# Kernel tuning notes

Hardware: AMD Instinct MI355X
Metric: run time of the kernel (lower is better)

## Reference

```python
import jax, jax.numpy as jnp
import numpy as np

B, N, D = 64, 1024, 128
K = 6  # hardcoded neighbor count in the module


def setup_inputs() -> dict:
    key = jax.random.key(0)
    ks = jax.random.split(key, 11)
    def lin(k, out_d, in_d):
        kw, kb = jax.random.split(k)
        s = 1.0 / np.sqrt(in_d)
        W = jax.random.uniform(kw, (out_d, in_d), minval=-s, maxval=s, dtype=jnp.float32)
        b = jax.random.uniform(kb, (out_d,), minval=-s, maxval=s, dtype=jnp.float32)
        return W, b
    loc = jax.random.uniform(ks[0], (B, N, 2), dtype=jnp.float32)
    deadline = jax.random.uniform(ks[1], (B, N), dtype=jnp.float32)
    depot = jax.random.uniform(ks[2], (B, 2), dtype=jnp.float32)
    W3d, b3d = lin(ks[3], D, 3)
    W2d, b2d = lin(ks[4], D, 2)
    Wnb, bnb = lin(ks[5], D, K * D)
    Wdep, bdep = lin(ks[6], D, 2)
    return {"loc": loc, "deadline": deadline, "depot": depot,
            "W3d": W3d, "b3d": b3d, "W2d": W2d, "b2d": b2d,
            "Wnb": Wnb, "bnb": bnb, "Wdep": Wdep, "bdep": bdep}


def reference(loc, deadline, depot, W3d, b3d, W2d, b2d, Wnb, bnb, Wdep, bdep):
    x = jnp.concatenate([loc, deadline[:, :, None]], axis=2)  # [B,N,3]
    x2 = x[:, :, 0:2]                                          # [B,N,2]
    F2 = jnp.einsum('bnf,df->bnd', x2, W2d) + b2d              # [B,N,D]
    F3 = jnp.einsum('bnf,df->bnd', x, W3d) + b3d               # [B,N,D]
    # pairwise euclidean distances; indices are non-differentiable -> stop_gradient
    diff = x2[:, None, :, :] - x2[:, :, None, :]               # [B,N,N,2]
    dist = jnp.sqrt(jnp.sum(diff * diff, axis=-1))             # [B,N,N]
    _, neighbors = jax.lax.top_k(jax.lax.stop_gradient(-dist), K)  # [B,N,K] smallest dists (incl. self)
    # faithful quirk: original does F0_embedding_2d[:, neighbors][0] == gather from batch-0 embeddings
    nb = F2[0][neighbors]                                      # [B,N,K,D]
    nb_c = nb.reshape(nb.shape[0], nb.shape[1], K * nb.shape[3])  # [B,N,K*D]
    Fn = jnp.einsum('bnf,df->bnd', nb_c, Wnb) + bnb            # [B,N,D]
    Ff = Fn + F3
    dep = depot @ Wdep.T + bdep                                 # [B,D]
    h = jax.nn.leaky_relu(jnp.concatenate([dep[:, None, :], Ff], axis=1), negative_slope=0.01)
    return h, h.mean(axis=1)
```

## Files before the change

### kernel.cpp

```cpp
#include <hip/hip_runtime.h>
#include <hip/hip_bf16.h>

#define CB 64
#define CN 1024
#define CD 128
#define CK 6

typedef __attribute__((ext_vector_type(8))) short short8;
typedef __attribute__((ext_vector_type(4))) float floatx4;

__device__ __forceinline__ unsigned short f2bf(float f) {
    union { float f; unsigned u; } c; c.f = f;
    unsigned u = c.u;
    u += 0x7FFFu + ((u >> 16) & 1u);
    return (unsigned short)(u >> 16);
}
__device__ __forceinline__ float bf2f(unsigned short u) {
    union { unsigned u; float f; } c; c.u = ((unsigned)u) << 16; return c.f;
}
__device__ __forceinline__ float bfe(const uint4& g, int dd) {
    unsigned w = (&g.x)[dd >> 1];
    unsigned short h = (dd & 1) ? (unsigned short)(w >> 16)
                                : (unsigned short)(w & 0xFFFFu);
    return bf2f(h);
}

#define WS_G      0
#define WS_NBRS   3145728
#define WS_IDS    3932160
#define WS_STARTS 4063232
#define WS_PART   4129024

struct SortSM { float2 pts[CN]; int cnt[256]; int base[256]; };
struct GSM    { unsigned short As[128 * 40]; unsigned short Bs[128 * 40]; };
union GridSM  { SortSM s; GSM g; };

__global__ void __launch_bounds__(256) k_gridg(
    const float* __restrict__ loc,
    const float* __restrict__ W2d,
    const float* __restrict__ b2d,
    const float* __restrict__ Wnb,
    unsigned short* __restrict__ ids,
    int* __restrict__ starts,
    unsigned short* __restrict__ G16)
{
    __shared__ GridSM sm;
    int t = threadIdx.x;

    if (blockIdx.x < 64) {
        int b = blockIdx.x;
        const float2* lb = (const float2*)loc + b * CN;
#pragma unroll
        for (int r = 0; r < 4; ++r) sm.s.pts[t + r * 256] = lb[t + r * 256];
        sm.s.cnt[t] = 0;
        __syncthreads();
        int mycell[4];
#pragma unroll
        for (int r = 0; r < 4; ++r) {
            float2 p = sm.s.pts[t * 4 + r];
            int cx = (int)(p.x * 16.0f); cx = cx > 15 ? 15 : cx;
            int cy = (int)(p.y * 16.0f); cy = cy > 15 ? 15 : cy;
            mycell[r] = (cy << 4) + cx;
            atomicAdd(&sm.s.cnt[mycell[r]], 1);
        }
        __syncthreads();
        for (int off = 1; off < 256; off <<= 1) {
            int u = (t >= off) ? sm.s.cnt[t - off] : 0;
            __syncthreads();
            sm.s.cnt[t] += u;
            __syncthreads();
        }
        int excl = (t == 0) ? 0 : sm.s.cnt[t - 1];
        sm.s.base[t] = excl;
        starts[b * 257 + t] = excl;
        if (t == 255) starts[b * 257 + 256] = sm.s.cnt[255];
        __syncthreads();
#pragma unroll
        for (int r = 0; r < 4; ++r) {
            int pos = atomicAdd(&sm.s.base[mycell[r]], 1);
            ids[b * CN + pos] = (unsigned short)(t * 4 + r);
        }
        return;
    }

    int gb = blockIdx.x - 64;
    int k = gb % 6;
    int tile = gb / 6;
    int n0 = tile << 7;

    int wave = t >> 6, lane = t & 63;
    int koff = (lane >> 4) * 8;
    int mrow = lane & 15;

    int e2 = t & 15, rg = t >> 4;
    float2 pl[8];
#pragma unroll
    for (int rr = 0; rr < 8; ++rr)
        pl[rr] = ((const float2*)loc)[n0 + rg + rr * 16];

    int bd = t >> 1, bhalf = t & 1;

    floatx4 acc[2][8];
#pragma unroll
    for (int i = 0; i < 2; ++i)
#pragma unroll
        for (int j = 0; j < 8; ++j) acc[i][j] = (floatx4){0.f, 0.f, 0.f, 0.f};

#pragma unroll
    for (int c = 0; c < 4; ++c) {
        __syncthreads();
        {
            int e0 = c * 32 + e2 * 2;
            float wx0 = W2d[e0 * 2],     wy0 = W2d[e0 * 2 + 1], bz0 = b2d[e0];
            float wx1 = W2d[e0 * 2 + 2], wy1 = W2d[e0 * 2 + 3], bz1 = b2d[e0 + 1];
#pragma unroll
            for (int rr = 0; rr < 8; ++rr) {
                float2 p = pl[rr];
                float v0 = fmaf(p.x, wx0, fmaf(p.y, wy0, bz0));
                float v1 = fmaf(p.x, wx1, fmaf(p.y, wy1, bz1));
                unsigned pack = (unsigned)f2bf(v0) | ((unsigned)f2bf(v1) << 16);
                *(unsigned*)&sm.g.As[(rg + rr * 16) * 40 + e2 * 2] = pack;
            }
        }
        {
            const float* src = Wnb + bd * 768 + k * 128 + c * 32 + bhalf * 16;
            float4 f0 = *(const float4*)(src);
            float4 f1 = *(const float4*)(src + 4);
            float4 f2v = *(const float4*)(src + 8);
            float4 f3 = *(const float4*)(src + 12);
            uint4 o0, o1;
            o0.x = (unsigned)f2bf(f0.x) | ((unsigned)f2bf(f0.y) << 16);
            o0.y = (unsigned)f2bf(f0.z) | ((unsigned)f2bf(f0.w) << 16);
            o0.z = (unsigned)f2bf(f1.x) | ((unsigned)f2bf(f1.y) << 16);
            o0.w = (unsigned)f2bf(f1.z) | ((unsigned)f2bf(f1.w) << 16);
            o1.x = (unsigned)f2bf(f2v.x) | ((unsigned)f2bf(f2v.y) << 16);
            o1.y = (unsigned)f2bf(f2v.z) | ((unsigned)f2bf(f2v.w) << 16);
            o1.z = (unsigned)f2bf(f3.x) | ((unsigned)f2bf(f3.y) << 16);
            o1.w = (unsigned)f2bf(f3.z) | ((unsigned)f2bf(f3.w) << 16);
            *(uint4*)&sm.g.Bs[bd * 40 + bhalf * 16] = o0;
            *(uint4*)&sm.g.Bs[bd * 40 + bhalf * 16 + 8] = o1;
        }
        __syncthreads();
        short8 af[2];
#pragma unroll
        for (int i = 0; i < 2; ++i)
            af[i] = *(const short8*)&sm.g.As[(wave * 32 + i * 16 + mrow) * 40 + koff];
#pragma unroll
        for (int j = 0; j < 8; ++j) {
            short8 bfr = *(const short8*)&sm.g.Bs[(j * 16 + mrow) * 40 + koff];
#pragma unroll
            for (int i = 0; i < 2; ++i)
                acc[i][j] = __builtin_amdgcn_mfma_f32_16x16x32_bf16(
                    af[i], bfr, acc[i][j], 0, 0, 0);
        }
    }

    int lq = lane >> 4, lc = lane & 15;
#pragma unroll
    for (int j = 0; j < 8; ++j) {
        int d = j * 16 + lc;
#pragma unroll
        for (int i = 0; i < 2; ++i) {
#pragma unroll
            for (int r = 0; r < 4; ++r) {
                int row = wave * 32 + i * 16 + lq * 4 + r;
                G16[(n0 + row) * 768 + k * 128 + d] = f2bf(acc[i][j][r]);
            }
        }
    }
}

__global__ void __launch_bounds__(256) k_knn(
    const float* __restrict__ loc,
    const unsigned short* __restrict__ ids,
    const int* __restrict__ starts,
    unsigned short* __restrict__ nbrs)
{
    __shared__ float2 xy_tmp[CN];
    __shared__ float2 xy_s[CN];
    __shared__ unsigned short ids_s[CN];
    __shared__ int st_s[257];
    int t = threadIdx.x;
    int b = blockIdx.x >> 4;
    int qbase = (blockIdx.x & 15) << 6;
    const float2* lb = (const float2*)loc + b * CN;
#pragma unroll
    for (int r = 0; r < 4; ++r) {
        int p = t + r * 256;
        xy_tmp[p] = lb[p];
        ids_s[p] = ids[b * CN + p];
    }
    st_s[t] = starts[b * 257 + t];
    if (t == 0) st_s[256] = starts[b * 257 + 256];
    __syncthreads();
#pragma unroll
    for (int r = 0; r < 4; ++r) {
        int p = t + r * 256;
        xy_s[p] = xy_tmp[ids_s[p]];
    }
    __syncthreads();

    int qp = qbase + (t >> 2);
    int pi = t & 3;
    int q = ids_s[qp];
    float2 qxy = xy_s[qp];
    float xq = qxy.x, yq = qxy.y;
    int cx = (int)(xq * 16.0f); cx = cx > 15 ? 15 : cx;
    int cy = (int)(yq * 16.0f); cy = cy > 15 ? 15 : cy;
    float dk[CK]; int ik[CK];
#pragma unroll
    for (int s = 0; s < CK; ++s) { dk[s] = 1e30f; ik[s] = 0x7FFFFFFF; }
    float dk5sq = __builtin_inff();
    const float h = 0.0625f;

#define KNN_CAND(P)                                                        \
    {                                                                      \
        float2 v = xy_s[P];                                                \
        float dx = __fsub_rn(v.x, xq);                                     \
        float dy = __fsub_rn(v.y, yq);                                     \
        float d2 = __fadd_rn(__fmul_rn(dx, dx), __fmul_rn(dy, dy));        \
        if (d2 < dk5sq) {                                                  \
            float ds = __fsqrt_rn(d2);                                     \
            int j = ids_s[P];                                              \
            if (ds < dk[CK - 1] || (ds == dk[CK - 1] && j < ik[CK - 1])) { \
                float dc = ds; int jc = j;                                 \
                _Pragma("unroll")                                          \
                for (int s = 0; s < CK; ++s) {                             \
                    bool sw = (dc < dk[s]) || (dc == dk[s] && jc < ik[s]); \
                    float od = dk[s]; int oi = ik[s];                      \
                    dk[s] = sw ? dc : od; ik[s] = sw ? jc : oi;            \
                    dc = sw ? od : dc;    jc = sw ? oi : jc;               \
                }                                                          \
                if (ik[CK - 1] != 0x7FFFFFFF)                              \
                    dk5sq = __fmul_rn(dk[CK - 1], dk[CK - 1]) * 1.000001f; \
            }                                                              \
        }                                                                  \
    }

    {
        int yl = cy > 0 ? cy - 1 : 0, yh = cy < 15 ? cy + 1 : 15;
        int xl = cx > 0 ? cx - 1 : 0, xh = cx < 15 ? cx + 1 : 15;
        for (int yy = yl; yy <= yh; ++yy) {
            int p  = st_s[(yy << 4) + xl] + pi;
            int pe = st_s[(yy << 4) + xh + 1];
            for (; p < pe; p += 4) KNN_CAND(p)
        }
    }
    bool done;
    {
        int x0 = cx - 1, x1 = cx + 1, y0 = cy - 1, y1 = cy + 1;
        done = (x0 <= 0 && y0 <= 0 && x1 >= 15 && y1 >= 15);
        float mL = x0 > 0  ? __fsub_rn(xq, (float)x0 * h)       : 1e30f;
        float mR = x1 < 15 ? __fsub_rn((float)(x1 + 1) * h, xq) : 1e30f;
        float mB = y0 > 0  ? __fsub_rn(yq, (float)y0 * h)       : 1e30f;
        float mT = y1 < 15 ? __fsub_rn((float)(y1 + 1) * h, yq) : 1e30f;
        float bound = fminf(fminf(mL, mR), fminf(mB, mT)) * 0.999999f;
        done = done || (ik[CK - 1] != 0x7FFFFFFF && dk[CK - 1] < bound);
    }
    if (!done) {
        for (int r = 2; r < 16; ++r) {
            int x0 = cx - r, x1 = cx + r, y0 = cy - r, y1 = cy + r;
            int yl = y0 < 0 ? 0 : y0, yh = y1 > 15 ? 15 : y1;
            int xl = x0 < 0 ? 0 : x0, xh = x1 > 15 ? 15 : x1;
            for (int yy = yl; yy <= yh; ++yy) {
                bool ey = (yy == y0) || (yy == y1);
                if (ey) {
                    int p  = st_s[(yy << 4) + xl] + pi;
                    int pe = st_s[(yy << 4) + xh + 1];
                    for (; p < pe; p += 4) KNN_CAND(p)
                } else {
                    if (x0 >= 0) {
                        int p  = st_s[(yy << 4) + x0] + pi;
                        int pe = st_s[(yy << 4) + x0 + 1];
                        for (; p < pe; p += 4) KNN_CAND(p)
                    }
                    if (x1 <= 15) {
                        int p  = st_s[(yy << 4) + x1] + pi;
                        int pe = st_s[(yy << 4) + x1 + 1];
                        for (; p < pe; p += 4) KNN_CAND(p)
                    }
                }
            }
            if (x0 <= 0 && y0 <= 0 && x1 >= 15 && y1 >= 15) break;
            float mL = x0 > 0  ? __fsub_rn(xq, (float)x0 * h)       : 1e30f;
            float mR = x1 < 15 ? __fsub_rn((float)(x1 + 1) * h, xq) : 1e30f;
            float mB = y0 > 0  ? __fsub_rn(yq, (float)y0 * h)       : 1e30f;
            float mT = y1 < 15 ? __fsub_rn((float)(y1 + 1) * h, yq) : 1e30f;
            float bound = fminf(fminf(mL, mR), fminf(mB, mT)) * 0.999999f;
            if (ik[CK - 1] != 0x7FFFFFFF && dk[CK - 1] < bound) break;
        }
    }
#undef KNN_CAND

#define KNN_MERGE(MASK)                                                     \
    {                                                                       \
        float od[CK]; int oi[CK];                                           \
        _Pragma("unroll")                                                   \
        for (int s = 0; s < CK; ++s) {                                      \
            od[s] = __shfl_xor(dk[s], MASK);                                \
            oi[s] = __shfl_xor(ik[s], MASK);                                \
        }                                                                   \
        _Pragma("unroll")                                                   \
        for (int e = 0; e < CK; ++e) {                                      \
            float dc = od[e]; int jc = oi[e];                               \
            if ((dc < dk[CK - 1]) || (dc == dk[CK - 1] && jc < ik[CK - 1])) { \
                _Pragma("unroll")                                           \
                for (int s = 0; s < CK; ++s) {                              \
                    bool sw = (dc < dk[s]) || (dc == dk[s] && jc < ik[s]);  \
                    float td = dk[s]; int ti = ik[s];                       \
                    dk[s] = sw ? dc : td; ik[s] = sw ? jc : ti;             \
                    dc = sw ? td : dc;    jc = sw ? ti : jc;                \
                }                                                           \
            }                                                               \
        }                                                                   \
    }
    KNN_MERGE(1)
    KNN_MERGE(2)
#undef KNN_MERGE

    if (pi == 0) {
        unsigned short* o = nbrs + (unsigned)(b * CN + q) * CK;
#pragma unroll
        for (int s = 0; s < CK; ++s) o[s] = (unsigned short)ik[s];
    }
}

__global__ void __launch_bounds__(256) k_gather(
    const float* __restrict__ loc,
    const float* __restrict__ dl,
    const unsigned short* __restrict__ nbrs,
    const unsigned short* __restrict__ ids,
    const unsigned short* __restrict__ G16,
    const float* __restrict__ W3d,
    const float* __restrict__ b3d,
    const float* __restrict__ bnb,
    float* __restrict__ outh,
    float* __restrict__ partials)
{
    __shared__ float psum[4][CD];
    __shared__ unsigned short nbs[64 * CK];
    __shared__ unsigned short nloc[64];
    int t = threadIdx.x, bx = blockIdx.x;
    int b = bx >> 4;
    int qbase = (bx & 15) << 6;

    if (t < 32)
        ((unsigned*)nloc)[t] = ((const unsigned*)(ids + b * CN + qbase))[t];
    __syncthreads();
    if (t < 64) {
        int n = nloc[t];
        const unsigned short* src = nbrs + ((size_t)(b << 10) + n) * CK;
#pragma unroll
        for (int s = 0; s < CK; ++s) nbs[t * CK + s] = src[s];
    }

    int d8 = t & 15, rg = t >> 4;
    int d0 = d8 * 8;
    float w0[8], w1[8], w2[8], bias[8];
#pragma unroll
    for (int dd = 0; dd < 8; ++dd) {
        int d = d0 + dd;
        w0[dd] = W3d[d * 3];
        w1[dd] = W3d[d * 3 + 1];
        w2[dd] = W3d[d * 3 + 2];
        bias[dd] = b3d[d] + bnb[d];
    }
    float csum[8];
#pragma unroll
    for (int dd = 0; dd < 8; ++dd) csum[dd] = 0.f;
    __syncthreads();

#pragma unroll
    for (int rr = 0; rr < 2; ++rr) {
        int r0 = rr * 32 + rg;
        int r1 = r0 + 16;
        int n0s = nloc[r0], n1s = nloc[r1];
        int gr0 = (b << 10) + n0s, gr1 = (b << 10) + n1s;
        const unsigned short* nA = nbs + r0 * CK;
        const unsigned short* nB = nbs + r1 * CK;
        uint4 ga0 = *(const uint4*)(G16 + nA[0] * 768 + 0 * 128 + d0);
        uint4 ga1 = *(const uint4*)(G16 + nA[1] * 768 + 1 * 128 + d0);
        uint4 ga2 = *(const uint4*)(G16 + nA[2] * 768 + 2 * 128 + d0);
        uint4 ga3 = *(const uint4*)(G16 + nA[3] * 768 + 3 * 128 + d0);
        uint4 ga4 = *(const uint4*)(G16 + nA[4] * 768 + 4 * 128 + d0);
        uint4 ga5 = *(const uint4*)(G16 + nA[5] * 768 + 5 * 128 + d0);
        uint4 gb0 = *(const uint4*)(G16 + nB[0] * 768 + 0 * 128 + d0);
        uint4 gb1 = *(const uint4*)(G16 + nB[1] * 768 + 1 * 128 + d0);
        uint4 gb2 = *(const uint4*)(G16 + nB[2] * 768 + 2 * 128 + d0);
        uint4 gb3 = *(const uint4*)(G16 + nB[3] * 768 + 3 * 128 + d0);
        uint4 gb4 = *(const uint4*)(G16 + nB[4] * 768 + 4 * 128 + d0);
        uint4 gb5 = *(const uint4*)(G16 + nB[5] * 768 + 5 * 128 + d0);
        float2 lA = ((const float2*)loc)[gr0];
        float2 lB = ((const float2*)loc)[gr1];
        float dA = dl[gr0];
        float dB = dl[gr1];
        {
            float o[8];
#pragma unroll
            for (int dd = 0; dd < 8; ++dd) {
                float a = ((((bfe(ga0, dd) + bfe(ga1, dd)) + bfe(ga2, dd))
                           + bfe(ga3, dd)) + bfe(ga4, dd)) + bfe(ga5, dd);
                float v = a + bias[dd] + lA.x * w0[dd] + lA.y * w1[dd]
                        + dA * w2[dd];
                o[dd] = v >= 0.f ? v : 0.01f * v;
                csum[dd] += o[dd];
            }
            float* ob = outh + ((long)b * 1025 + n0s + 1) * 128 + d0;
            float4 s0, s1;
            s0.x = o[0]; s0.y = o[1]; s0.z = o[2]; s0.w = o[3];
            s1.x = o[4]; s1.y = o[5]; s1.z = o[6]; s1.w = o[7];
            *(float4*)(ob) = s0;
            *(float4*)(ob + 4) = s1;
        }
        {
            float o[8];
#pragma unroll
            for (int dd = 0; dd < 8; ++dd) {
                float a = ((((bfe(gb0, dd) + bfe(gb1, dd)) + bfe(gb2, dd))
                           + bfe(gb3, dd)) + bfe(gb4, dd)) + bfe(gb5, dd);
                float v = a + bias[dd] + lB.x * w0[dd] + lB.y * w1[dd]
                        + dB * w2[dd];
                o[dd] = v >= 0.f ? v : 0.01f * v;
                csum[dd] += o[dd];
            }
            float* ob = outh + ((long)b * 1025 + n1s + 1) * 128 + d0;
            float4 s0, s1;
            s0.x = o[0]; s0.y = o[1]; s0.z = o[2]; s0.w = o[3];
            s1.x = o[4]; s1.y = o[5]; s1.z = o[6]; s1.w = o[7];
            *(float4*)(ob) = s0;
            *(float4*)(ob + 4) = s1;
        }
    }

#pragma unroll
    for (int dd = 0; dd < 8; ++dd) {
        csum[dd] += __shfl_xor(csum[dd], 16);
        csum[dd] += __shfl_xor(csum[dd], 32);
    }
    int wave = t >> 6, lane = t & 63;
    if (lane < 16) {
#pragma unroll
        for (int dd = 0; dd < 8; ++dd) psum[wave][d0 + dd] = csum[dd];
    }
    __syncthreads();
    if (t < CD)
        partials[(bx << 7) + t] =
            psum[0][t] + psum[1][t] + psum[2][t] + psum[3][t];
}

__global__ void k_fin(const float* __restrict__ depot,
                      const float* __restrict__ Wdep,
                      const float* __restrict__ bdep,
                      const float* __restrict__ partials,
                      float* __restrict__ out) {
    int idx = blockIdx.x * 256 + threadIdx.x;
    int b = idx >> 7, d = idx & 127;
    float acc = 0.f;
#pragma unroll
    for (int g = 0; g < 16; ++g) acc += partials[(b * 16 + g) * 128 + d];
    float dv = depot[b * 2] * Wdep[d * 2] + depot[b * 2 + 1] * Wdep[d * 2 + 1] + bdep[d];
    float lr = dv >= 0.f ? dv : 0.01f * dv;
    out[(long)b * 1025 * 128 + d] = lr;
    out[(long)CB * 1025 * 128 + idx] = (acc + lr) * (1.0f / 1025.0f);
}

extern "C" void kernel_launch(void* const* d_in, const int* in_sizes, int n_in,
                              void* d_out, int out_size, void* d_ws, size_t ws_size,
                              hipStream_t stream) {
    const float* loc      = (const float*)d_in[0];
    const float* deadline = (const float*)d_in[1];
    const float* depot    = (const float*)d_in[2];
    const float* W3d      = (const float*)d_in[3];
    const float* b3d      = (const float*)d_in[4];
    const float* W2d      = (const float*)d_in[5];
    const float* b2d      = (const float*)d_in[6];
    const float* Wnb      = (const float*)d_in[7];
    const float* bnb      = (const float*)d_in[8];
    const float* Wdep     = (const float*)d_in[9];
    const float* bdep     = (const float*)d_in[10];
    float* out = (float*)d_out;

    char* ws = (char*)d_ws;
    unsigned short* G16   = (unsigned short*)(ws + WS_G);
    unsigned short* nbrs  = (unsigned short*)(ws + WS_NBRS);
    unsigned short* ids   = (unsigned short*)(ws + WS_IDS);
    int* starts           = (int*)(ws + WS_STARTS);
    float* partials       = (float*)(ws + WS_PART);

    k_gridg<<<112, 256, 0, stream>>>(loc, W2d, b2d, Wnb, ids, starts, G16);
    k_knn<<<1024, 256, 0, stream>>>(loc, ids, starts, nbrs);
    k_gather<<<1024, 256, 0, stream>>>(loc, deadline, nbrs, ids, G16, W3d,
                                       b3d, bnb, out, partials);
    k_fin<<<32, 256, 0, stream>>>(depot, Wdep, bdep, partials, out);
}
```

Measured before the change: 134.0 us.

## Split each kNN query across 8 lanes and merge before the ring expansion

Each query point in the kNN kernel is now handled by 8 lanes instead of 4, so each block covers 32 queries and the grid doubles to 2048 blocks. The 8 lanes merge their partial top-6 lists right after the 3x3 cell scan. The early-exit bound and the pruning threshold are then computed from the merged result, so the ring expansion can stop sooner and skip more candidates. A dedup-aware merge handles the second round, since lanes already share the merged entries. In exchange, every block reloads and re-sorts the full batch's points into shared memory twice as often, and the extra shuffle-merge steps add cost.

```diff
diff --git a/kernel.cpp b/kernel.cpp
--- a/kernel.cpp
+++ b/kernel.cpp
@@ -181,8 +181,8 @@
     __shared__ unsigned short ids_s[CN];
     __shared__ int st_s[257];
     int t = threadIdx.x;
-    int b = blockIdx.x >> 4;
-    int qbase = (blockIdx.x & 15) << 6;
+    int b = blockIdx.x >> 5;
+    int qbase = (blockIdx.x & 31) << 5;
     const float2* lb = (const float2*)loc + b * CN;
 #pragma unroll
     for (int r = 0; r < 4; ++r) {
@@ -200,8 +200,8 @@
     }
     __syncthreads();
 
-    int qp = qbase + (t >> 2);
-    int pi = t & 3;
+    int qp = qbase + (t >> 3);
+    int pi = t & 7;
     int q = ids_s[qp];
     float2 qxy = xy_s[qp];
     float xq = qxy.x, yq = qxy.y;
@@ -237,61 +237,6 @@
         }                                                                  \
     }
 
-    {
-        int yl = cy > 0 ? cy - 1 : 0, yh = cy < 15 ? cy + 1 : 15;
-        int xl = cx > 0 ? cx - 1 : 0, xh = cx < 15 ? cx + 1 : 15;
-        for (int yy = yl; yy <= yh; ++yy) {
-            int p  = st_s[(yy << 4) + xl] + pi;
-            int pe = st_s[(yy << 4) + xh + 1];
-            for (; p < pe; p += 4) KNN_CAND(p)
-        }
-    }
-    bool done;
-    {
-        int x0 = cx - 1, x1 = cx + 1, y0 = cy - 1, y1 = cy + 1;
-        done = (x0 <= 0 && y0 <= 0 && x1 >= 15 && y1 >= 15);
-        float mL = x0 > 0  ? __fsub_rn(xq, (float)x0 * h)       : 1e30f;
-        float mR = x1 < 15 ? __fsub_rn((float)(x1 + 1) * h, xq) : 1e30f;
-        float mB = y0 > 0  ? __fsub_rn(yq, (float)y0 * h)       : 1e30f;
-        float mT = y1 < 15 ? __fsub_rn((float)(y1 + 1) * h, yq) : 1e30f;
-        float bound = fminf(fminf(mL, mR), fminf(mB, mT)) * 0.999999f;
-        done = done || (ik[CK - 1] != 0x7FFFFFFF && dk[CK - 1] < bound);
-    }
-    if (!done) {
-        for (int r = 2; r < 16; ++r) {
-            int x0 = cx - r, x1 = cx + r, y0 = cy - r, y1 = cy + r;
-            int yl = y0 < 0 ? 0 : y0, yh = y1 > 15 ? 15 : y1;
-            int xl = x0 < 0 ? 0 : x0, xh = x1 > 15 ? 15 : x1;
-            for (int yy = yl; yy <= yh; ++yy) {
-                bool ey = (yy == y0) || (yy == y1);
-                if (ey) {
-                    int p  = st_s[(yy << 4) + xl] + pi;
-                    int pe = st_s[(yy << 4) + xh + 1];
-                    for (; p < pe; p += 4) KNN_CAND(p)
-                } else {
-                    if (x0 >= 0) {
-                        int p  = st_s[(yy << 4) + x0] + pi;
-                        int pe = st_s[(yy << 4) + x0 + 1];
-                        for (; p < pe; p += 4) KNN_CAND(p)
-                    }
-                    if (x1 <= 15) {
-                        int p  = st_s[(yy << 4) + x1] + pi;
-                        int pe = st_s[(yy << 4) + x1 + 1];
-                        for (; p < pe; p += 4) KNN_CAND(p)
-                    }
-                }
-            }
-            if (x0 <= 0 && y0 <= 0 && x1 >= 15 && y1 >= 15) break;
-            float mL = x0 > 0  ? __fsub_rn(xq, (float)x0 * h)       : 1e30f;
-            float mR = x1 < 15 ? __fsub_rn((float)(x1 + 1) * h, xq) : 1e30f;
-            float mB = y0 > 0  ? __fsub_rn(yq, (float)y0 * h)       : 1e30f;
-            float mT = y1 < 15 ? __fsub_rn((float)(y1 + 1) * h, yq) : 1e30f;
-            float bound = fminf(fminf(mL, mR), fminf(mB, mT)) * 0.999999f;
-            if (ik[CK - 1] != 0x7FFFFFFF && dk[CK - 1] < bound) break;
-        }
-    }
-#undef KNN_CAND
-
 #define KNN_MERGE(MASK)                                                     \
     {                                                                       \
         float od[CK]; int oi[CK];                                           \
@@ -314,9 +259,101 @@
             }                                                               \
         }                                                                   \
     }
+
+#define KNN_MERGE_D(MASK)                                                   \
+    {                                                                       \
+        float od[CK]; int oi[CK];                                           \
+        _Pragma("unroll")                                                   \
+        for (int s = 0; s < CK; ++s) {                                      \
+            od[s] = __shfl_xor(dk[s], MASK);                                \
+            oi[s] = __shfl_xor(ik[s], MASK);                                \
+        }                                                                   \
+        _Pragma("unroll")                                                   \
+        for (int e = 0; e < CK; ++e) {                                      \
+            float dc = od[e]; int jc = oi[e];                               \
+            bool dup = false;                                               \
+            _Pragma("unroll")                                               \
+            for (int s = 0; s < CK; ++s) dup = dup || (jc == ik[s]);        \
+            if (!dup &&                                                     \
+                ((dc < dk[CK - 1]) || (dc == dk[CK - 1] && jc < ik[CK - 1]))) { \
+                _Pragma("unroll")                                           \
+                for (int s = 0; s < CK; ++s) {                              \
+                    bool sw = (dc < dk[s]) || (dc == dk[s] && jc < ik[s]);  \
+                    float td = dk[s]; int ti = ik[s];                       \
+                    dk[s] = sw ? dc : td; ik[s] = sw ? jc : ti;             \
+                    dc = sw ? td : dc;    jc = sw ? ti : jc;                \
+                }                                                           \
+            }                                                               \
+        }                                                                   \
+    }
+
+    {
+        int yl = cy > 0 ? cy - 1 : 0, yh = cy < 15 ? cy + 1 : 15;
+        int xl = cx > 0 ? cx - 1 : 0, xh = cx < 15 ? cx + 1 : 15;
+        for (int yy = yl; yy <= yh; ++yy) {
+            int p  = st_s[(yy << 4) + xl] + pi;
+            int pe = st_s[(yy << 4) + xh + 1];
+            for (; p < pe; p += 8) KNN_CAND(p)
+        }
+    }
+
     KNN_MERGE(1)
     KNN_MERGE(2)
+    KNN_MERGE(4)
+
+    bool done;
+    {
+        int x0 = cx - 1, x1 = cx + 1, y0 = cy - 1, y1 = cy + 1;
+        done = (x0 <= 0 && y0 <= 0 && x1 >= 15 && y1 >= 15);
+        float mL = x0 > 0  ? __fsub_rn(xq, (float)x0 * h)       : 1e30f;
+        float mR = x1 < 15 ? __fsub_rn((float)(x1 + 1) * h, xq) : 1e30f;
+        float mB = y0 > 0  ? __fsub_rn(yq, (float)y0 * h)       : 1e30f;
+        float mT = y1 < 15 ? __fsub_rn((float)(y1 + 1) * h, yq) : 1e30f;
+        float bound = fminf(fminf(mL, mR), fminf(mB, mT)) * 0.999999f;
+        done = done || (ik[CK - 1] != 0x7FFFFFFF && dk[CK - 1] < bound);
+    }
+
+    if (!done) {
+        if (ik[CK - 1] != 0x7FFFFFFF)
+            dk5sq = __fmul_rn(dk[CK - 1], dk[CK - 1]) * 1.000001f;
+        for (int r = 2; r < 16; ++r) {
+            int x0 = cx - r, x1 = cx + r, y0 = cy - r, y1 = cy + r;
+            int yl = y0 < 0 ? 0 : y0, yh = y1 > 15 ? 15 : y1;
+            int xl = x0 < 0 ? 0 : x0, xh = x1 > 15 ? 15 : x1;
+            for (int yy = yl; yy <= yh; ++yy) {
+                bool ey = (yy == y0) || (yy == y1);
+                if (ey) {
+                    int p  = st_s[(yy << 4) + xl] + pi;
+                    int pe = st_s[(yy << 4) + xh + 1];
+                    for (; p < pe; p += 8) KNN_CAND(p)
+                } else {
+                    if (x0 >= 0) {
+                        int p  = st_s[(yy << 4) + x0] + pi;
+                        int pe = st_s[(yy << 4) + x0 + 1];
+                        for (; p < pe; p += 8) KNN_CAND(p)
+                    }
+                    if (x1 <= 15) {
+                        int p  = st_s[(yy << 4) + x1] + pi;
+                        int pe = st_s[(yy << 4) + x1 + 1];
+                        for (; p < pe; p += 8) KNN_CAND(p)
+                    }
+                }
+            }
+            if (x0 <= 0 && y0 <= 0 && x1 >= 15 && y1 >= 15) break;
+            float mL = x0 > 0  ? __fsub_rn(xq, (float)x0 * h)       : 1e30f;
+            float mR = x1 < 15 ? __fsub_rn((float)(x1 + 1) * h, xq) : 1e30f;
+            float mB = y0 > 0  ? __fsub_rn(yq, (float)y0 * h)       : 1e30f;
+            float mT = y1 < 15 ? __fsub_rn((float)(y1 + 1) * h, yq) : 1e30f;
+            float bound = fminf(fminf(mL, mR), fminf(mB, mT)) * 0.999999f;
+            if (ik[CK - 1] != 0x7FFFFFFF && dk[CK - 1] < bound) break;
+        }
+        KNN_MERGE_D(1)
+        KNN_MERGE_D(2)
+        KNN_MERGE_D(4)
+    }
+#undef KNN_CAND
 #undef KNN_MERGE
+#undef KNN_MERGE_D
 
     if (pi == 0) {
         unsigned short* o = nbrs + (unsigned)(b * CN + q) * CK;
@@ -488,7 +525,7 @@
     float* partials       = (float*)(ws + WS_PART);
 
     k_gridg<<<112, 256, 0, stream>>>(loc, W2d, b2d, Wnb, ids, starts, G16);
-    k_knn<<<1024, 256, 0, stream>>>(loc, ids, starts, nbrs);
+    k_knn<<<2048, 256, 0, stream>>>(loc, ids, starts, nbrs);
     k_gather<<<1024, 256, 0, stream>>>(loc, deadline, nbrs, ids, G16, W3d,
                                        b3d, bnb, out, partials);
     k_fin<<<32, 256, 0, stream>>>(depot, Wdep, bdep, partials, out);
```

After: 130.8 us. -2.4%, faster.
